# Kernel optimization log

Hardware: AMD Instinct MI355X
Metric: run time of the kernel (lower is better)

Reference implementation:

```python
import jax, jax.numpy as jnp
import numpy as np
from jax import lax

B, C_IN, C_OUT, H, W, K, MID = 16, 256, 256, 64, 64, 3, 64
BN_EPS = 1e-5


def setup_inputs() -> dict:
    key = jax.random.key(0)
    ks = jax.random.split(key, 16)
    inp = {
        'x': jax.random.normal(ks[0], (B, C_IN, H, W), dtype=jnp.float32),
        # 4 kernel banks: (4, c2, c1//g, k, k)
        'weight': jax.random.normal(ks[1], (4, C_OUT, C_IN, K, K), dtype=jnp.float32) * 0.05,
        'gamma': jnp.ones((C_OUT,), jnp.float32),
        'beta': jnp.zeros((C_OUT,), jnp.float32),
    }
    # four attention branches: Linear(c, mid, bias=False) -> ReLU -> Linear(mid, 4, bias=True)
    names = ['s', 'c', 'f', 'w']
    for i, n in enumerate(names):
        inp[f'fc_{n}_w1'] = jax.random.normal(ks[2 + 3 * i], (MID, C_IN), dtype=jnp.float32) * 0.05
        inp[f'fc_{n}_w2'] = jax.random.normal(ks[3 + 3 * i], (4, MID), dtype=jnp.float32) * 0.05
        inp[f'fc_{n}_b2'] = jax.random.normal(ks[4 + 3 * i], (4,), dtype=jnp.float32) * 0.05
    return inp


def _branch(pooled, w1, w2, b2):
    # pooled: [B, C]; w1: [MID, C]; w2: [4, MID]
    h = jax.nn.relu(pooled @ w1.T)
    return jax.nn.softmax(h @ w2.T + b2, axis=1)  # [B, 4]


def reference(x, weight, gamma, beta,
              fc_s_w1, fc_s_w2, fc_s_b2,
              fc_c_w1, fc_c_w2, fc_c_b2,
              fc_f_w1, fc_f_w2, fc_f_b2,
              fc_w_w1, fc_w_w2, fc_w_b2):
    b = x.shape[0]
    pooled = jnp.mean(x, axis=(2, 3))  # GAP -> [B, C]
    alpha = (_branch(pooled, fc_s_w1, fc_s_w2, fc_s_b2)
             * _branch(pooled, fc_c_w1, fc_c_w2, fc_c_b2)
             * _branch(pooled, fc_f_w1, fc_f_w2, fc_f_b2)
             * _branch(pooled, fc_w_w1, fc_w_w2, fc_w_b2))  # [B, 4]
    # per-sample dynamic kernels: [B, out_c, in_c, k, k]
    dyn_w = jnp.einsum('bn,noikl->boikl', alpha, weight)

    def conv_one(xi, wi):
        # xi: [C, H, W]; wi: [out_c, in_c, k, k]
        return lax.conv_general_dilated(
            xi[None], wi, window_strides=(1, 1), padding='SAME',
            dimension_numbers=('NCHW', 'OIHW', 'NCHW'))[0]

    out = jax.vmap(conv_one)(x, dyn_w)  # [B, out_c, H, W]

    # BatchNorm2d (training-mode batch statistics)
    mean = jnp.mean(out, axis=(0, 2, 3))
    var = jnp.var(out, axis=(0, 2, 3))
    out = (out - mean[None, :, None, None]) * jax.lax.rsqrt(var + BN_EPS)[None, :, None, None]
    return out * gamma[None, :, None, None] + beta[None, :, None, None]
```

## Files before the change

kernel.cpp:

```cpp
#include <hip/hip_runtime.h>
#include <math.h>

#define BB 16
#define CIN 256
#define COUT 256
#define HH 64
#define WW 64
#define NBANK_STRIDE 589824

typedef short bf16x8 __attribute__((ext_vector_type(8)));
typedef float f32x4 __attribute__((ext_vector_type(4)));

#define WS_XT_OFF 32768
#define WS_DW_OFF 33587200
#define WS_NEED   52461568ULL

static __device__ __forceinline__ short f2bf(float f) {
    union { float f; unsigned u; } v; v.f = f;
    unsigned r = v.u + 0x7FFF + ((v.u >> 16) & 1);
    return (short)(r >> 16);
}

struct AttnParams {
    const float* w1[4];
    const float* w2[4];
    const float* b2[4];
};

__global__ __launch_bounds__(256) void zero_kernel(float* __restrict__ ws) {
    ws[blockIdx.x * 256 + threadIdx.x] = 0.f;
}

__global__ __launch_bounds__(256) void xpose_kernel(const float* __restrict__ x,
                                                    short* __restrict__ xT,
                                                    float* __restrict__ pooled) {
    const int ci0 = blockIdx.x * 32;
    const int h = blockIdx.y;
    const int b = blockIdx.z;
    const int t = threadIdx.x;
    __shared__ __align__(16) short tile[64][40];
    {
        const int ci = t >> 3;
        const int l = t & 7;
        const float4* src = (const float4*)(x + ((size_t)(b * 256 + ci0 + ci)) * 4096 + h * 64);
        float4 v1 = src[l * 2];
        float4 v2 = src[l * 2 + 1];
        tile[l * 8 + 0][ci] = f2bf(v1.x);
        tile[l * 8 + 1][ci] = f2bf(v1.y);
        tile[l * 8 + 2][ci] = f2bf(v1.z);
        tile[l * 8 + 3][ci] = f2bf(v1.w);
        tile[l * 8 + 4][ci] = f2bf(v2.x);
        tile[l * 8 + 5][ci] = f2bf(v2.y);
        tile[l * 8 + 6][ci] = f2bf(v2.z);
        tile[l * 8 + 7][ci] = f2bf(v2.w);
        float s = v1.x + v1.y + v1.z + v1.w + v2.x + v2.y + v2.z + v2.w;
        s += __shfl_xor(s, 1, 64);
        s += __shfl_xor(s, 2, 64);
        s += __shfl_xor(s, 4, 64);
        if (l == 0) atomicAdd(&pooled[b * 256 + ci0 + ci], s);
    }
    __syncthreads();
    {
        const int w = t >> 2;
        const int s = t & 3;
        bf16x8 val = *(const bf16x8*)&tile[w][s * 8];
        *(bf16x8*)&xT[((size_t)b * 4096 + h * 64 + w) * 256 + ci0 + s * 8] = val;
    }
}

__global__ __launch_bounds__(256) void attn_kernel(AttnParams p, float* __restrict__ ws_f) {
    const int b = blockIdx.x;
    const int t = threadIdx.x;
    const int wv = t >> 6;
    const int lane = t & 63;
    __shared__ float ps[256];
    __shared__ float hs[4][64];
    __shared__ float lg[4][4];
    __shared__ float sm[4][4];
    ws_f[4096 + b * 256 + t] = 0.f;
    ps[t] = ws_f[b * 256 + t] * (1.0f / 4096.0f);
    __syncthreads();
    {
        const float4* w1v = (const float4*)(p.w1[wv] + lane * 256);
        float h = 0.f;
#pragma unroll 8
        for (int i = 0; i < 64; ++i) {
            float4 w4 = w1v[i];
            h += w4.x * ps[i * 4 + 0] + w4.y * ps[i * 4 + 1] +
                 w4.z * ps[i * 4 + 2] + w4.w * ps[i * 4 + 3];
        }
        hs[wv][lane] = fmaxf(h, 0.f);
    }
    __syncthreads();
    if (t < 16) {
        const int n = t >> 2, j = t & 3;
        const float* w2 = p.w2[n];
        float l = p.b2[n][j];
        for (int m = 0; m < 64; ++m) l += w2[j * 64 + m] * hs[n][m];
        lg[n][j] = l;
    }
    __syncthreads();
    if (t < 4) {
        const int n = t;
        float mx = fmaxf(fmaxf(lg[n][0], lg[n][1]), fmaxf(lg[n][2], lg[n][3]));
        float e0 = expf(lg[n][0] - mx), e1 = expf(lg[n][1] - mx);
        float e2 = expf(lg[n][2] - mx), e3 = expf(lg[n][3] - mx);
        float inv = 1.f / (e0 + e1 + e2 + e3);
        sm[n][0] = e0 * inv; sm[n][1] = e1 * inv; sm[n][2] = e2 * inv; sm[n][3] = e3 * inv;
    }
    __syncthreads();
    if (t < 4) ws_f[b * 256 + t] = sm[0][t] * sm[1][t] * sm[2][t] * sm[3][t];
}

__global__ __launch_bounds__(256) void dynw_kernel(const float* __restrict__ wt,
                                                   const float* __restrict__ ws_f,
                                                   short* __restrict__ dynwT) {
    const int co = blockIdx.x;
    const int ci = threadIdx.x;
    float w[4][9];
#pragma unroll
    for (int n = 0; n < 4; ++n) {
        const size_t base = ((size_t)(n * 256 + co) * 256 + ci) * 9;
#pragma unroll
        for (int k = 0; k < 9; ++k) w[n][k] = wt[base + k];
    }
    for (int b = 0; b < BB; ++b) {
        const float a0 = ws_f[b * 256 + 0];
        const float a1 = ws_f[b * 256 + 1];
        const float a2 = ws_f[b * 256 + 2];
        const float a3 = ws_f[b * 256 + 3];
#pragma unroll
        for (int k = 0; k < 9; ++k) {
            float v = a0 * w[0][k] + a1 * w[1][k] + a2 * w[2][k] + a3 * w[3][k];
            dynwT[((size_t)(b * 9 + k) * 256 + co) * 256 + ci] = f2bf(v);
        }
    }
}

__global__ __launch_bounds__(256, 2) void conv_mfma_kernel(const short* __restrict__ xT,
                                                           const short* __restrict__ dynwT,
                                                           float* __restrict__ out,
                                                           float* __restrict__ bn_part) {
    const int nt = blockIdx.x;
    const int mt = blockIdx.y;
    const int b = blockIdx.z;
    const int t = threadIdx.x;
    const int lane = t & 63;
    const int wv = t >> 6;
    const int wx = wv & 1;
    const int wy = wv >> 1;
    const int mh = lane & 15;
    const int q = lane >> 4;
    const int r0 = nt * 4;
    const int co0 = mt * 128;

    __shared__ __align__(16) short xs[396 * 40];
    __shared__ __align__(16) short As[2][128 * 40];
    __shared__ float red[128][2][2];

    f32x4 acc[4][8];
#pragma unroll
    for (int i = 0; i < 4; ++i)
#pragma unroll
        for (int j = 0; j < 8; ++j) acc[i][j] = (f32x4){0.f, 0.f, 0.f, 0.f};

    const int arow0 = t >> 2;
    const int asub = t & 3;
    const short* Ab = dynwT + (size_t)b * 9 * 65536 + (co0 + arow0) * 256 + asub * 8;
    const int a_lds0 = arow0 * 40 + asub * 8;
    const int a_lds1 = (arow0 + 64) * 40 + asub * 8;
    const int a_rd = (wy * 64 + mh) * 40 + q * 8;

    const bf16x8 zero8 = {0, 0, 0, 0, 0, 0, 0, 0};

    for (int cc = 0; cc < 8; ++cc) {
        const int ci0 = cc * 32;
        __syncthreads();
        bf16x8 pa0 = *(const bf16x8*)(Ab + ci0);
        bf16x8 pa1 = *(const bf16x8*)(Ab + 64 * 256 + ci0);
#pragma unroll
        for (int i = 0; i < 7; ++i) {
            int idx = t + 256 * i;
            if (idx < 1584) {
                int p = idx >> 2;
                int sub = idx & 3;
                int lr = p / 66;
                int lc = p - lr * 66;
                int r = r0 - 1 + lr;
                int c = lc - 1;
                bf16x8 v = zero8;
                if ((unsigned)r < 64u && (unsigned)c < 64u)
                    v = *(const bf16x8*)&xT[((size_t)b * 4096 + r * 64 + c) * 256 + ci0 + sub * 8];
                *(bf16x8*)&xs[p * 40 + sub * 8] = v;
            }
        }
        *(bf16x8*)&As[0][a_lds0] = pa0;
        *(bf16x8*)&As[0][a_lds1] = pa1;
        __syncthreads();
#pragma unroll
        for (int khw = 0; khw < 9; ++khw) {
            const int kh = khw / 3;
            const int kw = khw - kh * 3;
            bf16x8 na0, na1;
            if (khw < 8) {
                na0 = *(const bf16x8*)(Ab + (khw + 1) * 65536 + ci0);
                na1 = *(const bf16x8*)(Ab + (khw + 1) * 65536 + 64 * 256 + ci0);
            }
            bf16x8 bfr[8];
#pragma unroll
            for (int ni = 0; ni < 8; ++ni) {
                const int row_l = wx * 2 + (ni >> 2) + kh;
                const int col_l = (ni & 3) * 16 + kw + mh;
                bfr[ni] = *(const bf16x8*)&xs[(row_l * 66 + col_l) * 40 + q * 8];
            }
#pragma unroll
            for (int mi = 0; mi < 4; ++mi) {
                bf16x8 af = *(const bf16x8*)&As[khw & 1][a_rd + mi * 640];
#pragma unroll
                for (int ni = 0; ni < 8; ++ni)
                    acc[mi][ni] = __builtin_amdgcn_mfma_f32_16x16x32_bf16(af, bfr[ni], acc[mi][ni], 0, 0, 0);
            }
            if (khw < 8) {
                *(bf16x8*)&As[(khw + 1) & 1][a_lds0] = na0;
                *(bf16x8*)&As[(khw + 1) & 1][a_lds1] = na1;
            }
            __syncthreads();
        }
    }

    float s16[4][4], q16[4][4];
#pragma unroll
    for (int mi = 0; mi < 4; ++mi)
#pragma unroll
        for (int reg = 0; reg < 4; ++reg) { s16[mi][reg] = 0.f; q16[mi][reg] = 0.f; }

#pragma unroll
    for (int mi = 0; mi < 4; ++mi) {
#pragma unroll
        for (int ni = 0; ni < 8; ++ni) {
            const int pix = wx * 128 + ni * 16 + mh;
            const int h = r0 + (pix >> 6);
            const int w = pix & 63;
#pragma unroll
            for (int reg = 0; reg < 4; ++reg) {
                const int co = co0 + wy * 64 + mi * 16 + q * 4 + reg;
                const float e = acc[mi][ni][reg];
                out[(((size_t)b * 256 + co) << 12) + (h << 6) + w] = e;
                s16[mi][reg] += e;
                q16[mi][reg] += e * e;
            }
        }
    }
#pragma unroll
    for (int mi = 0; mi < 4; ++mi)
#pragma unroll
        for (int reg = 0; reg < 4; ++reg) {
            float s = s16[mi][reg], sq = q16[mi][reg];
            s += __shfl_xor(s, 1, 64);  sq += __shfl_xor(sq, 1, 64);
            s += __shfl_xor(s, 2, 64);  sq += __shfl_xor(sq, 2, 64);
            s += __shfl_xor(s, 4, 64);  sq += __shfl_xor(sq, 4, 64);
            s += __shfl_xor(s, 8, 64);  sq += __shfl_xor(sq, 8, 64);
            if (mh == 0) {
                const int co_l = wy * 64 + mi * 16 + q * 4 + reg;
                red[co_l][0][wx] = s;
                red[co_l][1][wx] = sq;
            }
        }
    __syncthreads();
    {
        const int co_l = t >> 1;
        const int st = t & 1;
        float v = red[co_l][st][0] + red[co_l][st][1];
        atomicAdd(&bn_part[(st * 256 + co0 + co_l) * 8 + (nt & 7)], v);
    }
}

__global__ __launch_bounds__(256) void bn_finalize_kernel(const float* __restrict__ bn_part,
                                                          const float* __restrict__ gamma,
                                                          const float* __restrict__ beta,
                                                          float* __restrict__ scale,
                                                          float* __restrict__ shift) {
    const int co = threadIdx.x;
    float S = 0.f, Q = 0.f;
#pragma unroll
    for (int s = 0; s < 8; ++s) {
        S += bn_part[(co) * 8 + s];
        Q += bn_part[(256 + co) * 8 + s];
    }
    const float mean = S * (1.f / 65536.f);
    const float var = Q * (1.f / 65536.f) - mean * mean;
    const float inv = rsqrtf(var + 1e-5f);
    const float sc = gamma[co] * inv;
    scale[co] = sc;
    shift[co] = beta[co] - mean * sc;
}

__global__ __launch_bounds__(256) void bn_apply_kernel(float* __restrict__ out,
                                                       const float* __restrict__ scale,
                                                       const float* __restrict__ shift) {
    const int gid = blockIdx.x * 256 + threadIdx.x;
    const int c = (gid >> 10) & 255;
    float4* p = (float4*)out;
    float4 v = p[gid];
    const float sc = scale[c], sh = shift[c];
    v.x = v.x * sc + sh;
    v.y = v.y * sc + sh;
    v.z = v.z * sc + sh;
    v.w = v.w * sc + sh;
    p[gid] = v;
}

__global__ __launch_bounds__(256) void gap_kernel(const float* __restrict__ x,
                                                  float* __restrict__ pooled) {
    const int plane = blockIdx.x;
    const float4* p = (const float4*)(x + (size_t)plane * 4096);
    const int t = threadIdx.x;
    float s = 0.f;
#pragma unroll
    for (int i = 0; i < 4; ++i) {
        float4 v = p[t + 256 * i];
        s += v.x + v.y + v.z + v.w;
    }
#pragma unroll
    for (int off = 32; off > 0; off >>= 1) s += __shfl_down(s, off, 64);
    __shared__ float red[4];
    if ((t & 63) == 0) red[t >> 6] = s;
    __syncthreads();
    if (t == 0) pooled[plane] = (red[0] + red[1] + red[2] + red[3]) * (1.0f / 4096.0f);
}

__global__ __launch_bounds__(64) void attn64_kernel(const float* __restrict__ pooled,
                                                    AttnParams p,
                                                    float* __restrict__ alpha) {
    const int b = blockIdx.x;
    const int t = threadIdx.x;
    __shared__ float ps[256];
    __shared__ float hs[64];
    __shared__ float lg[4];
    __shared__ float prod[4];
#pragma unroll
    for (int i = 0; i < 4; ++i) ps[t + 64 * i] = pooled[b * 256 + t + 64 * i];
    if (t < 4) prod[t] = 1.f;
    __syncthreads();
    for (int n = 0; n < 4; ++n) {
        const float* w1 = p.w1[n];
        float h = 0.f;
        for (int c = 0; c < 256; ++c) h += w1[t * 256 + c] * ps[c];
        hs[t] = fmaxf(h, 0.f);
        __syncthreads();
        if (t < 4) {
            const float* w2 = p.w2[n];
            float l = p.b2[n][t];
            for (int m = 0; m < 64; ++m) l += w2[t * 64 + m] * hs[m];
            lg[t] = l;
        }
        __syncthreads();
        if (t == 0) {
            float mx = fmaxf(fmaxf(lg[0], lg[1]), fmaxf(lg[2], lg[3]));
            float e0 = expf(lg[0] - mx), e1 = expf(lg[1] - mx);
            float e2 = expf(lg[2] - mx), e3 = expf(lg[3] - mx);
            float inv = 1.f / (e0 + e1 + e2 + e3);
            prod[0] *= e0 * inv; prod[1] *= e1 * inv;
            prod[2] *= e2 * inv; prod[3] *= e3 * inv;
        }
        __syncthreads();
    }
    if (t < 4) alpha[b * 4 + t] = prod[t];
}

__global__ __launch_bounds__(256) void conv_fp32_kernel(const float* __restrict__ x,
                                                        const float* __restrict__ wt,
                                                        const float* __restrict__ alpha,
                                                        float* __restrict__ out) {
    const int h = blockIdx.x;
    const int cot = blockIdx.y;
    const int b = blockIdx.z;
    const int t = threadIdx.x;
    const int tx = t & 15;
    const int ty = t >> 4;
    const int co0 = cot * 64;
    __shared__ __align__(16) float xsf[32][68];
    __shared__ __align__(16) float wshf[3][32][68];
    const float a0 = alpha[b * 4 + 0], a1 = alpha[b * 4 + 1];
    const float a2 = alpha[b * 4 + 2], a3 = alpha[b * 4 + 3];
    float acc[4][4];
#pragma unroll
    for (int i = 0; i < 4; ++i)
#pragma unroll
        for (int j = 0; j < 4; ++j) acc[i][j] = 0.f;
    const size_t xbase = (size_t)b * CIN * 4096;
    for (int kh = 0; kh < 3; ++kh) {
        const int r = h + kh - 1;
        if (r < 0 || r >= HH) continue;
        for (int chunk = 0; chunk < 8; ++chunk) {
            const int ci0 = chunk * 32;
            __syncthreads();
#pragma unroll
            for (int i = 0; i < 8; ++i) {
                int flat = t + 256 * i;
                int ci = flat >> 6;
                int w = flat & 63;
                xsf[ci][1 + w] = x[xbase + (size_t)(ci0 + ci) * 4096 + r * 64 + w];
            }
            if (t < 32) { xsf[t][0] = 0.f; xsf[t][65] = 0.f; xsf[t][66] = 0.f; xsf[t][67] = 0.f; }
#pragma unroll
            for (int j = 0; j < 24; ++j) {
                int e = t + 256 * j;
                int co = e / 96;
                int rem = e - co * 96;
                int ci = rem / 3;
                int kw = rem - ci * 3;
                size_t g = (((size_t)(co0 + co) * 256 + (ci0 + ci)) * 3 + kh) * 3 + kw;
                wshf[kw][ci][co] = a0 * wt[g] + a1 * wt[g + NBANK_STRIDE] +
                                   a2 * wt[g + 2 * NBANK_STRIDE] + a3 * wt[g + 3 * NBANK_STRIDE];
            }
            __syncthreads();
            for (int ci = 0; ci < 32; ++ci) {
                float4 w0 = *(const float4*)&wshf[0][ci][tx * 4];
                float4 w1v = *(const float4*)&wshf[1][ci][tx * 4];
                float4 w2v = *(const float4*)&wshf[2][ci][tx * 4];
                float4 xa = *(const float4*)&xsf[ci][ty * 4];
                float4 xb = *(const float4*)&xsf[ci][ty * 4 + 4];
                float v[8] = {xa.x, xa.y, xa.z, xa.w, xb.x, xb.y, xb.z, xb.w};
                float aw[3][4] = {{w0.x, w0.y, w0.z, w0.w},
                                  {w1v.x, w1v.y, w1v.z, w1v.w},
                                  {w2v.x, w2v.y, w2v.z, w2v.w}};
#pragma unroll
                for (int kw = 0; kw < 3; ++kw)
#pragma unroll
                    for (int i = 0; i < 4; ++i)
#pragma unroll
                        for (int j = 0; j < 4; ++j)
                            acc[i][j] += aw[kw][i] * v[j + kw];
            }
        }
    }
    size_t obase = (((size_t)b * COUT + co0 + tx * 4) * 64 + h) * 64 + ty * 4;
#pragma unroll
    for (int i = 0; i < 4; ++i) {
        float4 o = {acc[i][0], acc[i][1], acc[i][2], acc[i][3]};
        *(float4*)&out[obase + (size_t)i * 4096] = o;
    }
}

__global__ __launch_bounds__(256) void bn_stats_kernel(const float* __restrict__ out,
                                                       const float* __restrict__ gamma,
                                                       const float* __restrict__ beta,
                                                       float* __restrict__ scale,
                                                       float* __restrict__ shift) {
    const int co = blockIdx.x;
    const int t = threadIdx.x;
    float s = 0.f, sq = 0.f;
    for (int b = 0; b < BB; ++b) {
        const float4* p = (const float4*)(out + ((size_t)b * 256 + co) * 4096);
#pragma unroll
        for (int i = 0; i < 4; ++i) {
            float4 v = p[t + 256 * i];
            s += v.x + v.y + v.z + v.w;
            sq += v.x * v.x + v.y * v.y + v.z * v.z + v.w * v.w;
        }
    }
#pragma unroll
    for (int off = 32; off > 0; off >>= 1) {
        s += __shfl_down(s, off, 64);
        sq += __shfl_down(sq, off, 64);
    }
    __shared__ float rs[4], rq[4];
    if ((t & 63) == 0) { rs[t >> 6] = s; rq[t >> 6] = sq; }
    __syncthreads();
    if (t == 0) {
        float S = rs[0] + rs[1] + rs[2] + rs[3];
        float Q = rq[0] + rq[1] + rq[2] + rq[3];
        float mean = S * (1.f / 65536.f);
        float var = Q * (1.f / 65536.f) - mean * mean;
        float inv = rsqrtf(var + 1e-5f);
        float sc = gamma[co] * inv;
        scale[co] = sc;
        shift[co] = beta[co] - mean * sc;
    }
}

extern "C" void kernel_launch(void* const* d_in, const int* in_sizes, int n_in,
                              void* d_out, int out_size, void* d_ws, size_t ws_size,
                              hipStream_t stream) {
    (void)in_sizes; (void)n_in; (void)out_size;
    const float* x = (const float*)d_in[0];
    const float* wt = (const float*)d_in[1];
    const float* gamma = (const float*)d_in[2];
    const float* beta = (const float*)d_in[3];
    AttnParams ap;
    for (int n = 0; n < 4; ++n) {
        ap.w1[n] = (const float*)d_in[4 + 3 * n];
        ap.w2[n] = (const float*)d_in[5 + 3 * n];
        ap.b2[n] = (const float*)d_in[6 + 3 * n];
    }
    float* ws_f = (float*)d_ws;
    float* out = (float*)d_out;

    if (ws_size >= WS_NEED) {
        short* xT = (short*)((char*)d_ws + WS_XT_OFF);
        short* dynwT = (short*)((char*)d_ws + WS_DW_OFF);
        float* bn_part = ws_f + 4096;
        float* scale = ws_f;
        float* shift = ws_f + 256;

        zero_kernel<<<16, 256, 0, stream>>>(ws_f);
        xpose_kernel<<<dim3(8, 64, 16), 256, 0, stream>>>(x, xT, ws_f);
        attn_kernel<<<16, 256, 0, stream>>>(ap, ws_f);
        dynw_kernel<<<256, 256, 0, stream>>>(wt, ws_f, dynwT);
        conv_mfma_kernel<<<dim3(16, 2, 16), 256, 0, stream>>>(xT, dynwT, out, bn_part);
        bn_finalize_kernel<<<1, 256, 0, stream>>>(bn_part, gamma, beta, scale, shift);
        bn_apply_kernel<<<16384, 256, 0, stream>>>(out, scale, shift);
    } else {
        float* pooled = ws_f;
        float* alpha = ws_f + 4096;
        float* scale = ws_f + 4160;
        float* shift = ws_f + 4416;
        gap_kernel<<<4096, 256, 0, stream>>>(x, pooled);
        attn64_kernel<<<16, 64, 0, stream>>>(pooled, ap, alpha);
        conv_fp32_kernel<<<dim3(64, 4, 16), 256, 0, stream>>>(x, wt, alpha, out);
        bn_stats_kernel<<<256, 256, 0, stream>>>(out, gamma, beta, scale, shift);
        bn_apply_kernel<<<16384, 256, 0, stream>>>(out, scale, shift);
    }
}
```

Measured before the change: 278.3 us.

## Load weight fragments directly into registers and remap blocks per XCD by batch

The weight (A) operand tiles are no longer staged through double-buffered LDS with a barrier per kernel tap. Each lane now loads its MFMA A fragments straight from global memory into registers and prefetches the next tap one step ahead. This removes nine __syncthreads per channel chunk and the LDS traffic for weights. The launch also becomes a 1D grid that places all blocks of the same batch sample on one XCD, to improve L2 reuse of that sample's weights and inputs. In exchange, weight loads are redundant across the two wx waves, each lane issues narrower strided global reads, and register pressure goes up.

```diff
diff --git a/kernel.cpp b/kernel.cpp
--- a/kernel.cpp
+++ b/kernel.cpp
@@ -141,9 +141,14 @@
                                                            const short* __restrict__ dynwT,
                                                            float* __restrict__ out,
                                                            float* __restrict__ bn_part) {
-    const int nt = blockIdx.x;
-    const int mt = blockIdx.y;
-    const int b = blockIdx.z;
+    const int id = blockIdx.x;
+    const int xcd = id & 7;
+    const int wi = id >> 3;
+    const int b = xcd + ((wi >> 5) << 3);
+    const int rem = wi & 31;
+    const int mt = rem >> 4;
+    const int nt = rem & 15;
+
     const int t = threadIdx.x;
     const int lane = t & 63;
     const int wv = t >> 6;
@@ -155,7 +160,6 @@
     const int co0 = mt * 128;
 
     __shared__ __align__(16) short xs[396 * 40];
-    __shared__ __align__(16) short As[2][128 * 40];
     __shared__ float red[128][2][2];
 
     f32x4 acc[4][8];
@@ -164,20 +168,18 @@
 #pragma unroll
         for (int j = 0; j < 8; ++j) acc[i][j] = (f32x4){0.f, 0.f, 0.f, 0.f};
 
-    const int arow0 = t >> 2;
-    const int asub = t & 3;
-    const short* Ab = dynwT + (size_t)b * 9 * 65536 + (co0 + arow0) * 256 + asub * 8;
-    const int a_lds0 = arow0 * 40 + asub * 8;
-    const int a_lds1 = (arow0 + 64) * 40 + asub * 8;
-    const int a_rd = (wy * 64 + mh) * 40 + q * 8;
+    const short* Aw = dynwT + (size_t)b * 9 * 65536 + (co0 + wy * 64 + mh) * 256 + q * 8;
+
+    bf16x8 afn[4];
+#pragma unroll
+    for (int mi = 0; mi < 4; ++mi)
+        afn[mi] = *(const bf16x8*)(Aw + mi * 4096);
 
     const bf16x8 zero8 = {0, 0, 0, 0, 0, 0, 0, 0};
 
     for (int cc = 0; cc < 8; ++cc) {
         const int ci0 = cc * 32;
         __syncthreads();
-        bf16x8 pa0 = *(const bf16x8*)(Ab + ci0);
-        bf16x8 pa1 = *(const bf16x8*)(Ab + 64 * 256 + ci0);
 #pragma unroll
         for (int i = 0; i < 7; ++i) {
             int idx = t + 256 * i;
@@ -194,17 +196,20 @@
                 *(bf16x8*)&xs[p * 40 + sub * 8] = v;
             }
         }
-        *(bf16x8*)&As[0][a_lds0] = pa0;
-        *(bf16x8*)&As[0][a_lds1] = pa1;
         __syncthreads();
 #pragma unroll
         for (int khw = 0; khw < 9; ++khw) {
             const int kh = khw / 3;
             const int kw = khw - kh * 3;
-            bf16x8 na0, na1;
-            if (khw < 8) {
-                na0 = *(const bf16x8*)(Ab + (khw + 1) * 65536 + ci0);
-                na1 = *(const bf16x8*)(Ab + (khw + 1) * 65536 + 64 * 256 + ci0);
+            bf16x8 af[4];
+#pragma unroll
+            for (int mi = 0; mi < 4; ++mi) af[mi] = afn[mi];
+            {
+                const int nkhw = (khw < 8) ? (khw + 1) : 0;
+                const int nci0 = (khw < 8) ? ci0 : ((ci0 + 32 < 256) ? ci0 + 32 : ci0);
+#pragma unroll
+                for (int mi = 0; mi < 4; ++mi)
+                    afn[mi] = *(const bf16x8*)(Aw + (size_t)nkhw * 65536 + mi * 4096 + nci0);
             }
             bf16x8 bfr[8];
 #pragma unroll
@@ -214,17 +219,10 @@
                 bfr[ni] = *(const bf16x8*)&xs[(row_l * 66 + col_l) * 40 + q * 8];
             }
 #pragma unroll
-            for (int mi = 0; mi < 4; ++mi) {
-                bf16x8 af = *(const bf16x8*)&As[khw & 1][a_rd + mi * 640];
+            for (int mi = 0; mi < 4; ++mi)
 #pragma unroll
                 for (int ni = 0; ni < 8; ++ni)
-                    acc[mi][ni] = __builtin_amdgcn_mfma_f32_16x16x32_bf16(af, bfr[ni], acc[mi][ni], 0, 0, 0);
-            }
-            if (khw < 8) {
-                *(bf16x8*)&As[(khw + 1) & 1][a_lds0] = na0;
-                *(bf16x8*)&As[(khw + 1) & 1][a_lds1] = na1;
-            }
-            __syncthreads();
+                    acc[mi][ni] = __builtin_amdgcn_mfma_f32_16x16x32_bf16(af[mi], bfr[ni], acc[mi][ni], 0, 0, 0);
         }
     }
 
@@ -508,7 +506,7 @@
         xpose_kernel<<<dim3(8, 64, 16), 256, 0, stream>>>(x, xT, ws_f);
         attn_kernel<<<16, 256, 0, stream>>>(ap, ws_f);
         dynw_kernel<<<256, 256, 0, stream>>>(wt, ws_f, dynwT);
-        conv_mfma_kernel<<<dim3(16, 2, 16), 256, 0, stream>>>(xT, dynwT, out, bn_part);
+        conv_mfma_kernel<<<512, 256, 0, stream>>>(xT, dynwT, out, bn_part);
         bn_finalize_kernel<<<1, 256, 0, stream>>>(bn_part, gamma, beta, scale, shift);
         bn_apply_kernel<<<16384, 256, 0, stream>>>(out, scale, shift);
     } else {
```

Result: slower. 321.1 us (+15.4%).
